# Optimization experiments

Hardware: AMD Instinct MI355X
Metric: run time of the kernel (lower is better)

The kernel has to match this reference:

```python
import jax, jax.numpy as jnp
import numpy as np

N = 100000   # num nodes
E = 1200000  # num edges
D = 64       # feature dim (input and both hidden layers)
R = 4        # num relations


def setup_inputs() -> dict:
    key = jax.random.key(0)
    ks = jax.random.split(key, 16)

    def p(k, shape, scale=0.05):
        return jax.random.normal(k, shape, dtype=jnp.float32) * scale

    inp = {
        "x": p(ks[0], (N, D), 1.0),
        "src": jax.random.randint(ks[1], (E,), 0, N),
        "dst": jax.random.randint(ks[2], (E,), 0, N),
        "rel": jax.random.randint(ks[3], (E,), 0, R),
    }
    i = 4
    for layer in (1, 2):
        inp[f"conv{layer}_w"] = p(ks[i], (D, R * D)); i += 1
        inp[f"conv{layer}_b"] = jnp.zeros((D,), jnp.float32)
        inp[f"conv{layer}_ws"] = p(ks[i], (D, D)); i += 1
        inp[f"conv{layer}_bs"] = jnp.zeros((D,), jnp.float32)
        inp[f"hw{layer}_pw"] = p(ks[i], (D, 2 * D)); i += 1
        inp[f"hw{layer}_pb"] = jnp.zeros((D,), jnp.float32)
        inp[f"hw{layer}_tw"] = p(ks[i], (D, 2 * D)); i += 1
        inp[f"hw{layer}_tb"] = jnp.full((D,), -2.0, jnp.float32)  # transform bias init -2
    return inp


def _rgc(x, src, dst, rel, w, b, ws, bs):
    # RelationalGraphConv: per-(node, relation) scatter-mean of source features,
    # then linear over concatenated relation slots + self-loop linear + sigmoid.
    msg = x[src]                                  # [E, D] gather
    seg = dst * R + rel                           # [E] flattened (node, relation) id
    s = jax.ops.segment_sum(msg, seg, num_segments=N * R)          # [N*R, D]
    cnt = jax.ops.segment_sum(jnp.ones((msg.shape[0], 1), msg.dtype), seg,
                              num_segments=N * R)                  # [N*R, 1]
    upd = (s / jnp.maximum(cnt, 1.0)).reshape(N, R * x.shape[1])   # [N, R*D]
    out = upd @ w.T + b + x @ ws.T + bs
    return jax.nn.sigmoid(out)


def _highway(h, prev, pw, pb, tw, tb):
    c = jnp.concatenate([h, prev], axis=1)        # [N, 2D]
    pr = jax.nn.relu(c @ pw.T + pb)
    g = jax.nn.sigmoid(c @ tw.T + tb)
    return g * pr + (1.0 - g) * h


def reference(x, src, dst, rel,
              conv1_w, conv1_b, conv1_ws, conv1_bs,
              hw1_pw, hw1_pb, hw1_tw, hw1_tb,
              conv2_w, conv2_b, conv2_ws, conv2_bs,
              hw2_pw, hw2_pb, hw2_tw, hw2_tb):
    h1 = _rgc(x, src, dst, rel, conv1_w, conv1_b, conv1_ws, conv1_bs)
    g1 = _highway(h1, x, hw1_pw, hw1_pb, hw1_tw, hw1_tb)   # prev_gcn = input
    h2 = _rgc(g1, src, dst, rel, conv2_w, conv2_b, conv2_ws, conv2_bs)
    g2 = _highway(h2, h1, hw2_pw, hw2_pb, hw2_tw, hw2_tb)  # prev_gcn = h1 (conv1 output)
    return g2  # node_feature, [N, D]
```

## Files before the change

### kernel.cpp

```cpp
#include <hip/hip_runtime.h>

#define NN 100000
#define NE 1200000
#define NRR 400000
#define NBIN 98
#define EPB 4096

typedef float f32x4 __attribute__((ext_vector_type(4)));
typedef __bf16 bf16x8 __attribute__((ext_vector_type(8)));

__device__ __forceinline__ float sigmoidf_(float x){ return 1.0f/(1.0f+__expf(-x)); }

__global__ __launch_bounds__(256)
void binhist_kernel(const int* __restrict__ dst, const int* __restrict__ rel,
                    int* __restrict__ bincnt){
  __shared__ int h[NBIN];
  int t = threadIdx.x;
  if (t < NBIN) h[t] = 0;
  __syncthreads();
  for (int e = blockIdx.x*256 + t; e < NE; e += 512*256){
    int bin = (dst[e]*4 + rel[e]) >> 12;
    atomicAdd(&h[bin], 1);
  }
  __syncthreads();
  if (t < NBIN && h[t]) atomicAdd(&bincnt[t], h[t]);
}

__global__ void binscan_kernel(const int* __restrict__ bincnt, int* __restrict__ binoff,
                               int* __restrict__ bincur, int* __restrict__ soff){
  if (threadIdx.x == 0){
    int s = 0;
    for (int i = 0; i < NBIN; ++i){ binoff[i] = s; bincur[i] = s; s += bincnt[i]; }
    binoff[NBIN] = NE;
    soff[NRR] = NE;
  }
}

__global__ __launch_bounds__(256)
void passA_kernel(const int* __restrict__ src, const int* __restrict__ dst,
                  const int* __restrict__ rel, int* __restrict__ bincur,
                  unsigned* __restrict__ ebin){
  __shared__ int h[NBIN], runbase[NBIN];
  int t = threadIdx.x;
  if (t < NBIN) h[t] = 0;
  __syncthreads();
  int lo = blockIdx.x*EPB, hi = min(lo + EPB, NE);
  for (int e = lo + t; e < hi; e += 256)
    atomicAdd(&h[(dst[e]*4 + rel[e]) >> 12], 1);
  __syncthreads();
  if (t < NBIN){
    runbase[t] = h[t] ? atomicAdd(&bincur[t], h[t]) : 0;
    h[t] = 0;
  }
  __syncthreads();
  for (int e = lo + t; e < hi; e += 256){
    int seg = dst[e]*4 + rel[e];
    int bin = seg >> 12;
    int p = runbase[bin] + atomicAdd(&h[bin], 1);
    ebin[p] = (unsigned)src[e] | ((unsigned)(seg & 4095) << 17);
  }
}

__global__ __launch_bounds__(1024)
void passB_kernel(const unsigned* __restrict__ ebin, const int* __restrict__ binoff,
                  int* __restrict__ soff, unsigned* __restrict__ ebuck){
  __shared__ int st[4096];
  __shared__ int wsum[16], wbase[16];
  const int bin = blockIdx.x;
  const int t = threadIdx.x;
  const int base = binoff[bin], end = binoff[bin+1];
  #pragma unroll
  for (int i = 0; i < 4; ++i) st[t*4 + i] = 0;
  __syncthreads();
  for (int e = base + t; e < end; e += 1024)
    atomicAdd(&st[(ebin[e] >> 17) & 4095], 1);
  __syncthreads();
  int h0 = st[t*4], h1 = st[t*4+1], h2 = st[t*4+2], h3 = st[t*4+3];
  int lsum = h0 + h1 + h2 + h3;
  int lane = t & 63, wv = t >> 6;
  int inc = lsum;
  #pragma unroll
  for (int o = 1; o < 64; o <<= 1){ int u = __shfl_up(inc, o); if (lane >= o) inc += u; }
  if (lane == 63) wsum[wv] = inc;
  __syncthreads();
  if (t == 0){ int s = 0; for (int i = 0; i < 16; ++i){ wbase[i] = s; s += wsum[i]; } }
  __syncthreads();
  int ex = base + wbase[wv] + (inc - lsum);
  int s0 = ex, s1 = ex + h0, s2 = s1 + h1, s3 = s2 + h2;
  st[t*4] = s0; st[t*4+1] = s1; st[t*4+2] = s2; st[t*4+3] = s3;
  int sg = bin*4096 + t*4;
  if (sg   < NRR) soff[sg]   = s0;
  if (sg+1 < NRR) soff[sg+1] = s1;
  if (sg+2 < NRR) soff[sg+2] = s2;
  if (sg+3 < NRR) soff[sg+3] = s3;
  __syncthreads();
  for (int e = base + t; e < end; e += 1024){
    unsigned u = ebin[e];
    int p = atomicAdd(&st[(u >> 17) & 4095], 1);
    ebuck[p] = u & 0x1FFFFu;
  }
}

__global__ void tobf16_kernel(const float* __restrict__ xf, __bf16* __restrict__ xb){
  int i = (blockIdx.x*256 + threadIdx.x)*8;
  if (i < NN*64){
    f32x4 a = *(const f32x4*)(xf + i);
    f32x4 b = *(const f32x4*)(xf + i + 4);
    bf16x8 r;
    r[0]=(__bf16)a[0]; r[1]=(__bf16)a[1]; r[2]=(__bf16)a[2]; r[3]=(__bf16)a[3];
    r[4]=(__bf16)b[0]; r[5]=(__bf16)b[1]; r[6]=(__bf16)b[2]; r[7]=(__bf16)b[3];
    *(bf16x8*)(xb + i) = r;
  }
}

__global__ void prep_kernel(const float* __restrict__ w,  const float* __restrict__ b,
                            const float* __restrict__ ws, const float* __restrict__ bs,
                            const float* __restrict__ pw, const float* __restrict__ pb,
                            const float* __restrict__ tw, const float* __restrict__ tb,
                            const float* __restrict__ w2,  const float* __restrict__ b2,
                            const float* __restrict__ ws2, const float* __restrict__ bs2,
                            const float* __restrict__ pw2, const float* __restrict__ pb2,
                            const float* __restrict__ tw2, const float* __restrict__ tb2,
                            __bf16* __restrict__ W1a, __bf16* __restrict__ W2a,
                            float* __restrict__ B1a, float* __restrict__ B2a,
                            __bf16* __restrict__ W1b, __bf16* __restrict__ W2b,
                            float* __restrict__ B1b, float* __restrict__ B2b){
  int i = blockIdx.x*256 + threadIdx.x;
  if (i < 64*320) {
    int e = i & 7, lane = (i >> 3) & 63, j = (i >> 9) & 3, kbi = i >> 11;
    int n = j*16 + (lane & 15);
    int k = kbi*32 + (lane >> 4)*8 + e;
    float va = (k < 256) ? w[n*256 + k]  : ws[n*64 + (k - 256)];
    float vb = (k < 256) ? w2[n*256 + k] : ws2[n*64 + (k - 256)];
    W1a[i] = (__bf16)va;
    W1b[i] = (__bf16)vb;
  }
  if (i < 128*128) {
    int e = i & 7, lane = (i >> 3) & 63, j = (i >> 9) & 7, kbi = i >> 12;
    int n = j*16 + (lane & 15);
    int k = kbi*32 + (lane >> 4)*8 + e;
    float va = (n < 64) ? pw[n*128 + k]  : tw[(n - 64)*128 + k];
    float vb = (n < 64) ? pw2[n*128 + k] : tw2[(n - 64)*128 + k];
    W2a[i] = (__bf16)va;
    W2b[i] = (__bf16)vb;
  }
  if (i < 64)  { B1a[i] = b[i] + bs[i];  B1b[i] = b2[i] + bs2[i]; }
  if (i < 128) { B2a[i] = (i < 64) ? pb[i] : tb[i-64];
                 B2b[i] = (i < 64) ? pb2[i] : tb2[i-64]; }
}

__global__ __launch_bounds__(256)
void gather_kernel(const unsigned* __restrict__ ebuck, const int* __restrict__ soff,
                   const __bf16* __restrict__ inb, __bf16* __restrict__ segb){
  const int sgg = blockIdx.x*32 + (threadIdx.x >> 3);
  const int fl  = threadIdx.x & 7;
  const int e0 = soff[sgg];
  const int e1 = soff[sgg + 1];
  const int c  = e1 - e0;

  f32x4 a0 = {0.f,0.f,0.f,0.f}, a1 = {0.f,0.f,0.f,0.f};
  f32x4 b0 = {0.f,0.f,0.f,0.f}, b1 = {0.f,0.f,0.f,0.f};
  int i = 0;
  for (; i + 2 <= c; i += 2){
    int s0 = (int)ebuck[e0 + i];
    int s1 = (int)ebuck[e0 + i + 1];
    bf16x8 v0 = *(const bf16x8*)(&inb[(size_t)s0*64 + fl*8]);
    bf16x8 v1 = *(const bf16x8*)(&inb[(size_t)s1*64 + fl*8]);
    a0[0]+=(float)v0[0]; a0[1]+=(float)v0[1]; a0[2]+=(float)v0[2]; a0[3]+=(float)v0[3];
    a1[0]+=(float)v0[4]; a1[1]+=(float)v0[5]; a1[2]+=(float)v0[6]; a1[3]+=(float)v0[7];
    b0[0]+=(float)v1[0]; b0[1]+=(float)v1[1]; b0[2]+=(float)v1[2]; b0[3]+=(float)v1[3];
    b1[0]+=(float)v1[4]; b1[1]+=(float)v1[5]; b1[2]+=(float)v1[6]; b1[3]+=(float)v1[7];
  }
  if (i < c){
    int s0 = (int)ebuck[e0 + i];
    bf16x8 v0 = *(const bf16x8*)(&inb[(size_t)s0*64 + fl*8]);
    a0[0]+=(float)v0[0]; a0[1]+=(float)v0[1]; a0[2]+=(float)v0[2]; a0[3]+=(float)v0[3];
    a1[0]+=(float)v0[4]; a1[1]+=(float)v0[5]; a1[2]+=(float)v0[6]; a1[3]+=(float)v0[7];
  }
  float inv = 1.0f / fmaxf((float)c, 1.0f);
  bf16x8 r;
  r[0]=(__bf16)((a0[0]+b0[0])*inv); r[1]=(__bf16)((a0[1]+b0[1])*inv);
  r[2]=(__bf16)((a0[2]+b0[2])*inv); r[3]=(__bf16)((a0[3]+b0[3])*inv);
  r[4]=(__bf16)((a1[0]+b1[0])*inv); r[5]=(__bf16)((a1[1]+b1[1])*inv);
  r[6]=(__bf16)((a1[2]+b1[2])*inv); r[7]=(__bf16)((a1[3]+b1[3])*inv);

  const int n   = sgg >> 2, rr = sgg & 3;
  const int nb  = n >> 4,  ml = n & 15;
  const int kbi = rr*2 + (fl >> 2);
  const int kgs = fl & 3;
  *(bf16x8*)(&segb[(size_t)((nb*8 + kbi)*64 + kgs*16 + ml)*8]) = r;
}

#define HSP 72

template<bool LAYER1>
__global__ __launch_bounds__(256, 4)
void dense_kernel(const __bf16* __restrict__ segbs,
                  const __bf16* __restrict__ xinb,
                  const __bf16* __restrict__ prevb,
                  const __bf16* __restrict__ W1s,
                  const __bf16* __restrict__ W2s,
                  const float* __restrict__ bias1,
                  const float* __restrict__ bias2,
                  __bf16* __restrict__ hb,
                  __bf16* __restrict__ gb,
                  float* __restrict__ outp)
{
  __shared__ __align__(16) __bf16 hs[64*HSP];
  __shared__ __align__(16) float outs[64*64];

  const int tid  = threadIdx.x;
  const int lane = tid & 63;
  const int wv   = tid >> 6;
  const int mloc = lane & 15;
  const int kg   = lane >> 4;
  const int wb   = blockIdx.x*64 + wv*16;
  const int arow = min(wb + mloc, NN-1);
  const int nbq  = min(wb, NN-16) >> 4;
  const size_t abase = (size_t)nbq * (8*512);

  f32x4 acc1[4] = {};

  #pragma unroll
  for (int kbi = 0; kbi < 8; ++kbi) {
    bf16x8 af = *(const bf16x8*)(&segbs[abase + (size_t)(kbi*64 + lane)*8]);
    #pragma unroll
    for (int j = 0; j < 4; ++j) {
      bf16x8 bf = *(const bf16x8*)(&W1s[((kbi*4 + j)*64 + lane)*8]);
      acc1[j] = __builtin_amdgcn_mfma_f32_16x16x32_bf16(af, bf, acc1[j], 0,0,0);
    }
  }
  #pragma unroll
  for (int kb = 0; kb < 64; kb += 32) {
    bf16x8 af = *(const bf16x8*)(&xinb[(size_t)arow*64 + kb + kg*8]);
    const int kbi = 8 + (kb >> 5);
    #pragma unroll
    for (int j = 0; j < 4; ++j) {
      bf16x8 bf = *(const bf16x8*)(&W1s[((kbi*4 + j)*64 + lane)*8]);
      acc1[j] = __builtin_amdgcn_mfma_f32_16x16x32_bf16(af, bf, acc1[j], 0,0,0);
    }
  }

  #pragma unroll
  for (int j = 0; j < 4; ++j) {
    int col = j*16 + mloc;
    float b1 = bias1[col];
    #pragma unroll
    for (int r = 0; r < 4; ++r) {
      float hv = sigmoidf_(acc1[j][r] + b1);
      acc1[j][r] = hv;
      hs[(wv*16 + kg*4 + r)*HSP + col] = (__bf16)hv;
    }
  }

  if (LAYER1) {
    #pragma unroll
    for (int i = 0; i < 2; ++i) {
      int r2 = i*8 + (lane >> 3);
      int c2 = lane & 7;
      bf16x8 v = *(const bf16x8*)(&hs[(wv*16 + r2)*HSP + c2*8]);
      int grow = wb + r2;
      if (grow < NN) *(bf16x8*)(&hb[(size_t)grow*64 + c2*8]) = v;
    }
  }

  f32x4 acc2[8] = {};
  #pragma unroll
  for (int kb = 0; kb < 64; kb += 32) {
    bf16x8 af = *(const bf16x8*)(&hs[(wv*16 + mloc)*HSP + kb + kg*8]);
    const int kbi = kb >> 5;
    #pragma unroll
    for (int j = 0; j < 8; ++j) {
      bf16x8 bf = *(const bf16x8*)(&W2s[((kbi*8 + j)*64 + lane)*8]);
      acc2[j] = __builtin_amdgcn_mfma_f32_16x16x32_bf16(af, bf, acc2[j], 0,0,0);
    }
  }
  #pragma unroll
  for (int kb = 0; kb < 64; kb += 32) {
    bf16x8 af = *(const bf16x8*)(&prevb[(size_t)arow*64 + kb + kg*8]);
    const int kbi = 2 + (kb >> 5);
    #pragma unroll
    for (int j = 0; j < 8; ++j) {
      bf16x8 bf = *(const bf16x8*)(&W2s[((kbi*8 + j)*64 + lane)*8]);
      acc2[j] = __builtin_amdgcn_mfma_f32_16x16x32_bf16(af, bf, acc2[j], 0,0,0);
    }
  }

  #pragma unroll
  for (int j = 0; j < 4; ++j) {
    int col = j*16 + mloc;
    float bp = bias2[col];
    float bt = bias2[64 + col];
    #pragma unroll
    for (int r = 0; r < 4; ++r) {
      float pr = fmaxf(acc2[j][r] + bp, 0.0f);
      float g  = sigmoidf_(acc2[j+4][r] + bt);
      float hv = acc1[j][r];
      float ov = g*pr + (1.0f - g)*hv;
      if (LAYER1) {
        hs[(wv*16 + kg*4 + r)*HSP + col] = (__bf16)ov;
      } else {
        outs[(wv*16 + kg*4 + r)*64 + col] = ov;
      }
    }
  }
  if (LAYER1) {
    #pragma unroll
    for (int i = 0; i < 2; ++i) {
      int r2 = i*8 + (lane >> 3);
      int c2 = lane & 7;
      bf16x8 v = *(const bf16x8*)(&hs[(wv*16 + r2)*HSP + c2*8]);
      int grow = wb + r2;
      if (grow < NN) *(bf16x8*)(&gb[(size_t)grow*64 + c2*8]) = v;
    }
  } else {
    #pragma unroll
    for (int i = 0; i < 4; ++i) {
      int pos = i*256 + lane*4;
      int r2 = pos >> 6, c2 = pos & 63;
      int grow = wb + r2;
      if (grow < NN)
        *(f32x4*)(&outp[(size_t)grow*64 + c2]) =
            *(const f32x4*)(&outs[(wv*16 + r2)*64 + c2]);
    }
  }
}

extern "C" void kernel_launch(void* const* d_in, const int* in_sizes, int n_in,
                              void* d_out, int out_size, void* d_ws, size_t ws_size,
                              hipStream_t stream){
  const float* x    = (const float*)d_in[0];
  const int*   src  = (const int*)d_in[1];
  const int*   dst  = (const int*)d_in[2];
  const int*   rel  = (const int*)d_in[3];
  const float* c1w  = (const float*)d_in[4];
  const float* c1b  = (const float*)d_in[5];
  const float* c1ws = (const float*)d_in[6];
  const float* c1bs = (const float*)d_in[7];
  const float* h1pw = (const float*)d_in[8];
  const float* h1pb = (const float*)d_in[9];
  const float* h1tw = (const float*)d_in[10];
  const float* h1tb = (const float*)d_in[11];
  const float* c2w  = (const float*)d_in[12];
  const float* c2b  = (const float*)d_in[13];
  const float* c2ws = (const float*)d_in[14];
  const float* c2bs = (const float*)d_in[15];
  const float* h2pw = (const float*)d_in[16];
  const float* h2pb = (const float*)d_in[17];
  const float* h2tw = (const float*)d_in[18];
  const float* h2tb = (const float*)d_in[19];

  char* p = (char*)d_ws;
  __bf16* segb = (__bf16*)p;  p += (size_t)NRR*64*2;
  __bf16* xb   = (__bf16*)p;  p += (size_t)NN*64*2;
  __bf16* h1b  = (__bf16*)p;  p += (size_t)NN*64*2;
  __bf16* g1b  = (__bf16*)p;  p += (size_t)NN*64*2;
  unsigned* ebuck = (unsigned*)p; p += (size_t)NE*4;
  unsigned* ebin  = (unsigned*)p; p += (size_t)NE*4;
  int* soff    = (int*)p;     p += (size_t)(NRR+8)*4;
  int* bincnt  = (int*)p;     p += 128*4;
  int* binoff  = (int*)p;     p += 128*4;
  int* bincur  = (int*)p;     p += 128*4;
  __bf16* W1a  = (__bf16*)p;  p += 64*320*2;
  __bf16* W2a  = (__bf16*)p;  p += 128*128*2;
  __bf16* W1b  = (__bf16*)p;  p += 64*320*2;
  __bf16* W2b  = (__bf16*)p;  p += 128*128*2;
  float* B1a   = (float*)p;   p += 64*4;
  float* B2a   = (float*)p;   p += 128*4;
  float* B1b   = (float*)p;   p += 64*4;
  float* B2b   = (float*)p;   p += 128*4;

  float* out = (float*)d_out;

  hipMemsetAsync(bincnt, 0, 128*4, stream);
  binhist_kernel<<<512, 256, 0, stream>>>(dst, rel, bincnt);
  binscan_kernel<<<1, 64, 0, stream>>>(bincnt, binoff, bincur, soff);
  passA_kernel<<<(NE+EPB-1)/EPB, 256, 0, stream>>>(src, dst, rel, bincur, ebin);
  passB_kernel<<<NBIN, 1024, 0, stream>>>(ebin, binoff, soff, ebuck);

  tobf16_kernel<<<(NN*64/8 + 255)/256, 256, 0, stream>>>(x, xb);
  prep_kernel<<<80, 256, 0, stream>>>(c1w, c1b, c1ws, c1bs, h1pw, h1pb, h1tw, h1tb,
                                      c2w, c2b, c2ws, c2bs, h2pw, h2pb, h2tw, h2tb,
                                      W1a, W2a, B1a, B2a, W1b, W2b, B1b, B2b);

  gather_kernel<<<NRR/32, 256, 0, stream>>>(ebuck, soff, xb, segb);
  dense_kernel<true><<<(NN+63)/64, 256, 0, stream>>>(segb, xb, xb, W1a, W2a, B1a, B2a,
                                                     h1b, g1b, nullptr);
  gather_kernel<<<NRR/32, 256, 0, stream>>>(ebuck, soff, g1b, segb);
  dense_kernel<false><<<(NN+63)/64, 256, 0, stream>>>(segb, g1b, h1b, W1b, W2b, B1b, B2b,
                                                      nullptr, nullptr, out);
}
```

Baseline: 298.4 us.

## Replace two-pass bin sort with global atomic counting sort, fuse prep kernels

Replaces the binning radix-style sort (binscan, passA, passB) with a per-segment global histogram built in binhist, a block-wise exclusive scan producing offsets and cursors, and a scatter kernel that places each edge via a global atomic on its segment cursor. The bf16 conversion and weight-prep kernels are merged into one launch, and the gather kernel preloads the first eight edge indices up front to raise memory-level parallelism. This cuts launches and one full pass over the edge array, at the cost of 1.2M contended global atomics and a non-deterministic edge order within each segment.

```diff
diff --git a/kernel.cpp b/kernel.cpp
--- a/kernel.cpp
+++ b/kernel.cpp
@@ -4,7 +4,6 @@
 #define NE 1200000
 #define NRR 400000
 #define NBIN 98
-#define EPB 4096
 
 typedef float f32x4 __attribute__((ext_vector_type(4)));
 typedef __bf16 bf16x8 __attribute__((ext_vector_type(8)));
@@ -13,69 +12,36 @@
 
 __global__ __launch_bounds__(256)
 void binhist_kernel(const int* __restrict__ dst, const int* __restrict__ rel,
-                    int* __restrict__ bincnt){
+                    int* __restrict__ bincnt, int* __restrict__ scnt){
   __shared__ int h[NBIN];
   int t = threadIdx.x;
   if (t < NBIN) h[t] = 0;
   __syncthreads();
   for (int e = blockIdx.x*256 + t; e < NE; e += 512*256){
-    int bin = (dst[e]*4 + rel[e]) >> 12;
-    atomicAdd(&h[bin], 1);
+    int seg = dst[e]*4 + rel[e];
+    atomicAdd(&scnt[seg], 1);
+    atomicAdd(&h[seg >> 12], 1);
   }
   __syncthreads();
   if (t < NBIN && h[t]) atomicAdd(&bincnt[t], h[t]);
 }
 
-__global__ void binscan_kernel(const int* __restrict__ bincnt, int* __restrict__ binoff,
-                               int* __restrict__ bincur, int* __restrict__ soff){
-  if (threadIdx.x == 0){
-    int s = 0;
-    for (int i = 0; i < NBIN; ++i){ binoff[i] = s; bincur[i] = s; s += bincnt[i]; }
-    binoff[NBIN] = NE;
-    soff[NRR] = NE;
-  }
-}
-
-__global__ __launch_bounds__(256)
-void passA_kernel(const int* __restrict__ src, const int* __restrict__ dst,
-                  const int* __restrict__ rel, int* __restrict__ bincur,
-                  unsigned* __restrict__ ebin){
-  __shared__ int h[NBIN], runbase[NBIN];
-  int t = threadIdx.x;
-  if (t < NBIN) h[t] = 0;
-  __syncthreads();
-  int lo = blockIdx.x*EPB, hi = min(lo + EPB, NE);
-  for (int e = lo + t; e < hi; e += 256)
-    atomicAdd(&h[(dst[e]*4 + rel[e]) >> 12], 1);
-  __syncthreads();
-  if (t < NBIN){
-    runbase[t] = h[t] ? atomicAdd(&bincur[t], h[t]) : 0;
-    h[t] = 0;
-  }
-  __syncthreads();
-  for (int e = lo + t; e < hi; e += 256){
-    int seg = dst[e]*4 + rel[e];
-    int bin = seg >> 12;
-    int p = runbase[bin] + atomicAdd(&h[bin], 1);
-    ebin[p] = (unsigned)src[e] | ((unsigned)(seg & 4095) << 17);
-  }
-}
-
 __global__ __launch_bounds__(1024)
-void passB_kernel(const unsigned* __restrict__ ebin, const int* __restrict__ binoff,
-                  int* __restrict__ soff, unsigned* __restrict__ ebuck){
-  __shared__ int st[4096];
-  __shared__ int wsum[16], wbase[16];
+void segscan_kernel(const int* __restrict__ bincnt, const int* __restrict__ scnt,
+                    int* __restrict__ soff, int* __restrict__ scur){
+  __shared__ int bc[NBIN];
+  __shared__ int wsum[16], wbase[16], bb;
   const int bin = blockIdx.x;
   const int t = threadIdx.x;
-  const int base = binoff[bin], end = binoff[bin+1];
-  #pragma unroll
-  for (int i = 0; i < 4; ++i) st[t*4 + i] = 0;
-  __syncthreads();
-  for (int e = base + t; e < end; e += 1024)
-    atomicAdd(&st[(ebin[e] >> 17) & 4095], 1);
-  __syncthreads();
-  int h0 = st[t*4], h1 = st[t*4+1], h2 = st[t*4+2], h3 = st[t*4+3];
+  if (t < NBIN) bc[t] = bincnt[t];
+  __syncthreads();
+  if (t == 0){ int s = 0; for (int i = 0; i < bin; ++i) s += bc[i]; bb = s; }
+  __syncthreads();
+  const int sg = bin*4096 + t*4;
+  int h0=0,h1=0,h2=0,h3=0;
+  if (sg < NRR){
+    h0 = scnt[sg]; h1 = scnt[sg+1]; h2 = scnt[sg+2]; h3 = scnt[sg+3];
+  }
   int lsum = h0 + h1 + h2 + h3;
   int lane = t & 63, wv = t >> 6;
   int inc = lsum;
@@ -85,47 +51,55 @@
   __syncthreads();
   if (t == 0){ int s = 0; for (int i = 0; i < 16; ++i){ wbase[i] = s; s += wsum[i]; } }
   __syncthreads();
-  int ex = base + wbase[wv] + (inc - lsum);
+  int ex = bb + wbase[wv] + (inc - lsum);
   int s0 = ex, s1 = ex + h0, s2 = s1 + h1, s3 = s2 + h2;
-  st[t*4] = s0; st[t*4+1] = s1; st[t*4+2] = s2; st[t*4+3] = s3;
-  int sg = bin*4096 + t*4;
-  if (sg   < NRR) soff[sg]   = s0;
-  if (sg+1 < NRR) soff[sg+1] = s1;
-  if (sg+2 < NRR) soff[sg+2] = s2;
-  if (sg+3 < NRR) soff[sg+3] = s3;
-  __syncthreads();
-  for (int e = base + t; e < end; e += 1024){
-    unsigned u = ebin[e];
-    int p = atomicAdd(&st[(u >> 17) & 4095], 1);
-    ebuck[p] = u & 0x1FFFFu;
-  }
-}
-
-__global__ void tobf16_kernel(const float* __restrict__ xf, __bf16* __restrict__ xb){
-  int i = (blockIdx.x*256 + threadIdx.x)*8;
-  if (i < NN*64){
-    f32x4 a = *(const f32x4*)(xf + i);
-    f32x4 b = *(const f32x4*)(xf + i + 4);
-    bf16x8 r;
-    r[0]=(__bf16)a[0]; r[1]=(__bf16)a[1]; r[2]=(__bf16)a[2]; r[3]=(__bf16)a[3];
-    r[4]=(__bf16)b[0]; r[5]=(__bf16)b[1]; r[6]=(__bf16)b[2]; r[7]=(__bf16)b[3];
-    *(bf16x8*)(xb + i) = r;
-  }
-}
-
-__global__ void prep_kernel(const float* __restrict__ w,  const float* __restrict__ b,
-                            const float* __restrict__ ws, const float* __restrict__ bs,
-                            const float* __restrict__ pw, const float* __restrict__ pb,
-                            const float* __restrict__ tw, const float* __restrict__ tb,
-                            const float* __restrict__ w2,  const float* __restrict__ b2,
-                            const float* __restrict__ ws2, const float* __restrict__ bs2,
-                            const float* __restrict__ pw2, const float* __restrict__ pb2,
-                            const float* __restrict__ tw2, const float* __restrict__ tb2,
-                            __bf16* __restrict__ W1a, __bf16* __restrict__ W2a,
-                            float* __restrict__ B1a, float* __restrict__ B2a,
-                            __bf16* __restrict__ W1b, __bf16* __restrict__ W2b,
-                            float* __restrict__ B1b, float* __restrict__ B2b){
-  int i = blockIdx.x*256 + threadIdx.x;
+  if (sg < NRR){
+    soff[sg] = s0; soff[sg+1] = s1; soff[sg+2] = s2; soff[sg+3] = s3;
+    scur[sg] = s0; scur[sg+1] = s1; scur[sg+2] = s2; scur[sg+3] = s3;
+  }
+  if (bin == NBIN-1 && t == 0) soff[NRR] = NE;
+}
+
+__global__ __launch_bounds__(256)
+void scatter_kernel(const int* __restrict__ src, const int* __restrict__ dst,
+                    const int* __restrict__ rel, int* __restrict__ scur,
+                    unsigned* __restrict__ ebuck){
+  int e = blockIdx.x*256 + threadIdx.x;
+  if (e < NE){
+    int seg = dst[e]*4 + rel[e];
+    int p = atomicAdd(&scur[seg], 1);
+    ebuck[p] = (unsigned)src[e];
+  }
+}
+
+#define TBB 3125
+__global__ __launch_bounds__(256)
+void tobf16_prep_kernel(const float* __restrict__ xf, __bf16* __restrict__ xb,
+                        const float* __restrict__ w,  const float* __restrict__ b,
+                        const float* __restrict__ ws, const float* __restrict__ bs,
+                        const float* __restrict__ pw, const float* __restrict__ pb,
+                        const float* __restrict__ tw, const float* __restrict__ tb,
+                        const float* __restrict__ w2,  const float* __restrict__ b2,
+                        const float* __restrict__ ws2, const float* __restrict__ bs2,
+                        const float* __restrict__ pw2, const float* __restrict__ pb2,
+                        const float* __restrict__ tw2, const float* __restrict__ tb2,
+                        __bf16* __restrict__ W1a, __bf16* __restrict__ W2a,
+                        float* __restrict__ B1a, float* __restrict__ B2a,
+                        __bf16* __restrict__ W1b, __bf16* __restrict__ W2b,
+                        float* __restrict__ B1b, float* __restrict__ B2b){
+  if (blockIdx.x < TBB) {
+    int i = (blockIdx.x*256 + threadIdx.x)*8;
+    if (i < NN*64){
+      f32x4 a = *(const f32x4*)(xf + i);
+      f32x4 c = *(const f32x4*)(xf + i + 4);
+      bf16x8 r;
+      r[0]=(__bf16)a[0]; r[1]=(__bf16)a[1]; r[2]=(__bf16)a[2]; r[3]=(__bf16)a[3];
+      r[4]=(__bf16)c[0]; r[5]=(__bf16)c[1]; r[6]=(__bf16)c[2]; r[7]=(__bf16)c[3];
+      *(bf16x8*)(xb + i) = r;
+    }
+    return;
+  }
+  int i = (blockIdx.x - TBB)*256 + threadIdx.x;
   if (i < 64*320) {
     int e = i & 7, lane = (i >> 3) & 63, j = (i >> 9) & 3, kbi = i >> 11;
     int n = j*16 + (lane & 15);
@@ -158,24 +132,36 @@
   const int e1 = soff[sgg + 1];
   const int c  = e1 - e0;
 
+  int idx[8];
+  #pragma unroll
+  for (int k = 0; k < 8; ++k) idx[k] = (int)ebuck[e0 + k];
+
   f32x4 a0 = {0.f,0.f,0.f,0.f}, a1 = {0.f,0.f,0.f,0.f};
   f32x4 b0 = {0.f,0.f,0.f,0.f}, b1 = {0.f,0.f,0.f,0.f};
-  int i = 0;
-  for (; i + 2 <= c; i += 2){
-    int s0 = (int)ebuck[e0 + i];
-    int s1 = (int)ebuck[e0 + i + 1];
-    bf16x8 v0 = *(const bf16x8*)(&inb[(size_t)s0*64 + fl*8]);
-    bf16x8 v1 = *(const bf16x8*)(&inb[(size_t)s1*64 + fl*8]);
-    a0[0]+=(float)v0[0]; a0[1]+=(float)v0[1]; a0[2]+=(float)v0[2]; a0[3]+=(float)v0[3];
-    a1[0]+=(float)v0[4]; a1[1]+=(float)v0[5]; a1[2]+=(float)v0[6]; a1[3]+=(float)v0[7];
-    b0[0]+=(float)v1[0]; b0[1]+=(float)v1[1]; b0[2]+=(float)v1[2]; b0[3]+=(float)v1[3];
-    b1[0]+=(float)v1[4]; b1[1]+=(float)v1[5]; b1[2]+=(float)v1[6]; b1[3]+=(float)v1[7];
-  }
-  if (i < c){
+  #pragma unroll
+  for (int k = 0; k < 8; ++k) {
+    if (k < c) {
+      bf16x8 v = *(const bf16x8*)(&inb[(size_t)idx[k]*64 + fl*8]);
+      if (k & 1) {
+        b0[0]+=(float)v[0]; b0[1]+=(float)v[1]; b0[2]+=(float)v[2]; b0[3]+=(float)v[3];
+        b1[0]+=(float)v[4]; b1[1]+=(float)v[5]; b1[2]+=(float)v[6]; b1[3]+=(float)v[7];
+      } else {
+        a0[0]+=(float)v[0]; a0[1]+=(float)v[1]; a0[2]+=(float)v[2]; a0[3]+=(float)v[3];
+        a1[0]+=(float)v[4]; a1[1]+=(float)v[5]; a1[2]+=(float)v[6]; a1[3]+=(float)v[7];
+      }
+    }
+  }
+  for (int i = 8; i < c; i += 2) {
     int s0 = (int)ebuck[e0 + i];
     bf16x8 v0 = *(const bf16x8*)(&inb[(size_t)s0*64 + fl*8]);
     a0[0]+=(float)v0[0]; a0[1]+=(float)v0[1]; a0[2]+=(float)v0[2]; a0[3]+=(float)v0[3];
     a1[0]+=(float)v0[4]; a1[1]+=(float)v0[5]; a1[2]+=(float)v0[6]; a1[3]+=(float)v0[7];
+    if (i + 1 < c) {
+      int s1 = (int)ebuck[e0 + i + 1];
+      bf16x8 v1 = *(const bf16x8*)(&inb[(size_t)s1*64 + fl*8]);
+      b0[0]+=(float)v1[0]; b0[1]+=(float)v1[1]; b0[2]+=(float)v1[2]; b0[3]+=(float)v1[3];
+      b1[0]+=(float)v1[4]; b1[1]+=(float)v1[5]; b1[2]+=(float)v1[6]; b1[3]+=(float)v1[7];
+    }
   }
   float inv = 1.0f / fmaxf((float)c, 1.0f);
   bf16x8 r;
@@ -355,12 +341,11 @@
   __bf16* xb   = (__bf16*)p;  p += (size_t)NN*64*2;
   __bf16* h1b  = (__bf16*)p;  p += (size_t)NN*64*2;
   __bf16* g1b  = (__bf16*)p;  p += (size_t)NN*64*2;
-  unsigned* ebuck = (unsigned*)p; p += (size_t)NE*4;
-  unsigned* ebin  = (unsigned*)p; p += (size_t)NE*4;
+  unsigned* ebuck = (unsigned*)p; p += (size_t)(NE+16)*4;
+  int* scnt    = (int*)p;     p += (size_t)(NRR+4096)*4;
+  int* bincnt  = (int*)p;     p += 128*4;
   int* soff    = (int*)p;     p += (size_t)(NRR+8)*4;
-  int* bincnt  = (int*)p;     p += 128*4;
-  int* binoff  = (int*)p;     p += 128*4;
-  int* bincur  = (int*)p;     p += 128*4;
+  int* scur    = (int*)p;     p += (size_t)NRR*4;
   __bf16* W1a  = (__bf16*)p;  p += 64*320*2;
   __bf16* W2a  = (__bf16*)p;  p += 128*128*2;
   __bf16* W1b  = (__bf16*)p;  p += 64*320*2;
@@ -372,14 +357,13 @@
 
   float* out = (float*)d_out;
 
-  hipMemsetAsync(bincnt, 0, 128*4, stream);
-  binhist_kernel<<<512, 256, 0, stream>>>(dst, rel, bincnt);
-  binscan_kernel<<<1, 64, 0, stream>>>(bincnt, binoff, bincur, soff);
-  passA_kernel<<<(NE+EPB-1)/EPB, 256, 0, stream>>>(src, dst, rel, bincur, ebin);
-  passB_kernel<<<NBIN, 1024, 0, stream>>>(ebin, binoff, soff, ebuck);
-
-  tobf16_kernel<<<(NN*64/8 + 255)/256, 256, 0, stream>>>(x, xb);
-  prep_kernel<<<80, 256, 0, stream>>>(c1w, c1b, c1ws, c1bs, h1pw, h1pb, h1tw, h1tb,
+  hipMemsetAsync(scnt, 0, ((size_t)(NRR+4096) + 128)*4, stream);
+  binhist_kernel<<<512, 256, 0, stream>>>(dst, rel, bincnt, scnt);
+  segscan_kernel<<<NBIN, 1024, 0, stream>>>(bincnt, scnt, soff, scur);
+  scatter_kernel<<<(NE+255)/256, 256, 0, stream>>>(src, dst, rel, scur, ebuck);
+
+  tobf16_prep_kernel<<<TBB+80, 256, 0, stream>>>(x, xb,
+                                      c1w, c1b, c1ws, c1bs, h1pw, h1pb, h1tw, h1tb,
                                       c2w, c2b, c2ws, c2bs, h2pw, h2pb, h2tw, h2tb,
                                       W1a, W2a, B1a, B2a, W1b, W2b, B1b, B2b);
 
```

Result: slower. 374.5 us (+25.5%).

## Fuse sort and prep kernels into one cooperative kernel with grid syncs

Applied to the files above, without the earlier changes.

Merges the bin histogram, bin scan, pass A scatter, pass B per-bin sort, bf16 conversion of x and weight packing into a single cooperative kernel of 98 blocks of 1024 threads, using grid-wide syncs in place of separate launches and a memset. Per-block partial histograms are written out and every block reduces and scans them redundantly. The aim is to remove launch overhead and inter-kernel gaps, at the cost of running the edge passes on only 98 blocks, which may underuse the GPU compared with the earlier wider grids.

```diff
diff --git a/kernel.cpp b/kernel.cpp
--- a/kernel.cpp
+++ b/kernel.cpp
@@ -1,74 +1,126 @@
 #include <hip/hip_runtime.h>
+#include <hip/hip_cooperative_groups.h>
+
+namespace cg = cooperative_groups;
 
 #define NN 100000
 #define NE 1200000
 #define NRR 400000
 #define NBIN 98
-#define EPB 4096
+#define CEPB 12245
 
 typedef float f32x4 __attribute__((ext_vector_type(4)));
 typedef __bf16 bf16x8 __attribute__((ext_vector_type(8)));
 
 __device__ __forceinline__ float sigmoidf_(float x){ return 1.0f/(1.0f+__expf(-x)); }
 
-__global__ __launch_bounds__(256)
-void binhist_kernel(const int* __restrict__ dst, const int* __restrict__ rel,
-                    int* __restrict__ bincnt){
-  __shared__ int h[NBIN];
-  int t = threadIdx.x;
-  if (t < NBIN) h[t] = 0;
-  __syncthreads();
-  for (int e = blockIdx.x*256 + t; e < NE; e += 512*256){
-    int bin = (dst[e]*4 + rel[e]) >> 12;
-    atomicAdd(&h[bin], 1);
-  }
-  __syncthreads();
-  if (t < NBIN && h[t]) atomicAdd(&bincnt[t], h[t]);
-}
-
-__global__ void binscan_kernel(const int* __restrict__ bincnt, int* __restrict__ binoff,
-                               int* __restrict__ bincur, int* __restrict__ soff){
-  if (threadIdx.x == 0){
+__global__ __launch_bounds__(1024)
+void sortprep_kernel(const int* __restrict__ src, const int* __restrict__ dst,
+                     const int* __restrict__ rel,
+                     const float* __restrict__ xf, __bf16* __restrict__ xb,
+                     const float* __restrict__ w,  const float* __restrict__ b,
+                     const float* __restrict__ ws, const float* __restrict__ bs,
+                     const float* __restrict__ pw, const float* __restrict__ pb,
+                     const float* __restrict__ tw, const float* __restrict__ tb,
+                     const float* __restrict__ w2,  const float* __restrict__ b2,
+                     const float* __restrict__ ws2, const float* __restrict__ bs2,
+                     const float* __restrict__ pw2, const float* __restrict__ pb2,
+                     const float* __restrict__ tw2, const float* __restrict__ tb2,
+                     __bf16* __restrict__ W1a, __bf16* __restrict__ W2a,
+                     float* __restrict__ B1a, float* __restrict__ B2a,
+                     __bf16* __restrict__ W1b, __bf16* __restrict__ W2b,
+                     float* __restrict__ B1b, float* __restrict__ B2b,
+                     int* __restrict__ hpart,
+                     unsigned* __restrict__ ebin, int* __restrict__ bincur,
+                     int* __restrict__ soff, unsigned* __restrict__ ebuck)
+{
+  cg::grid_group grid = cg::this_grid();
+  __shared__ int st[4096];
+  __shared__ int aux[NBIN + 2];
+  __shared__ int wsum[16], wbase[16];
+
+  const int t   = threadIdx.x;
+  const int bid = blockIdx.x;
+  const int lo  = bid*CEPB, hi = min(lo + CEPB, NE);
+
+  if (t < 128) st[t] = 0;
+  __syncthreads();
+  for (int e = lo + t; e < hi; e += 1024)
+    atomicAdd(&st[(dst[e]*4 + rel[e]) >> 12], 1);
+
+  for (int i = (bid*1024 + t)*8; i < NN*64; i += NBIN*1024*8){
+    f32x4 a = *(const f32x4*)(xf + i);
+    f32x4 c = *(const f32x4*)(xf + i + 4);
+    bf16x8 r;
+    r[0]=(__bf16)a[0]; r[1]=(__bf16)a[1]; r[2]=(__bf16)a[2]; r[3]=(__bf16)a[3];
+    r[4]=(__bf16)c[0]; r[5]=(__bf16)c[1]; r[6]=(__bf16)c[2]; r[7]=(__bf16)c[3];
+    *(bf16x8*)(xb + i) = r;
+  }
+  {
+    int i = bid*1024 + t;
+    if (i < 64*320) {
+      int e = i & 7, lane = (i >> 3) & 63, j = (i >> 9) & 3, kbi = i >> 11;
+      int n = j*16 + (lane & 15);
+      int k = kbi*32 + (lane >> 4)*8 + e;
+      float va = (k < 256) ? w[n*256 + k]  : ws[n*64 + (k - 256)];
+      float vb = (k < 256) ? w2[n*256 + k] : ws2[n*64 + (k - 256)];
+      W1a[i] = (__bf16)va;
+      W1b[i] = (__bf16)vb;
+    }
+    if (i < 128*128) {
+      int e = i & 7, lane = (i >> 3) & 63, j = (i >> 9) & 7, kbi = i >> 12;
+      int n = j*16 + (lane & 15);
+      int k = kbi*32 + (lane >> 4)*8 + e;
+      float va = (n < 64) ? pw[n*128 + k]  : tw[(n - 64)*128 + k];
+      float vb = (n < 64) ? pw2[n*128 + k] : tw2[(n - 64)*128 + k];
+      W2a[i] = (__bf16)va;
+      W2b[i] = (__bf16)vb;
+    }
+    if (i < 64)  { B1a[i] = b[i] + bs[i];  B1b[i] = b2[i] + bs2[i]; }
+    if (i < 128) { B2a[i] = (i < 64) ? pb[i] : tb[i-64];
+                   B2b[i] = (i < 64) ? pb2[i] : tb2[i-64]; }
+    if (i == 0) soff[NRR] = NE;
+  }
+  __syncthreads();
+  if (t < NBIN) hpart[bid*NBIN + t] = st[t];
+
+  grid.sync();
+
+  if (t < NBIN) {
     int s = 0;
-    for (int i = 0; i < NBIN; ++i){ binoff[i] = s; bincur[i] = s; s += bincnt[i]; }
-    binoff[NBIN] = NE;
-    soff[NRR] = NE;
-  }
-}
-
-__global__ __launch_bounds__(256)
-void passA_kernel(const int* __restrict__ src, const int* __restrict__ dst,
-                  const int* __restrict__ rel, int* __restrict__ bincur,
-                  unsigned* __restrict__ ebin){
-  __shared__ int h[NBIN], runbase[NBIN];
-  int t = threadIdx.x;
-  if (t < NBIN) h[t] = 0;
-  __syncthreads();
-  int lo = blockIdx.x*EPB, hi = min(lo + EPB, NE);
-  for (int e = lo + t; e < hi; e += 256)
-    atomicAdd(&h[(dst[e]*4 + rel[e]) >> 12], 1);
+    for (int k = 0; k < NBIN; ++k) s += hpart[k*NBIN + t];
+    st[t] = s;
+  }
+  __syncthreads();
+  if (t == 0) {
+    int s = 0;
+    for (int i = 0; i < NBIN; ++i){ aux[i] = s; s += st[i]; }
+    aux[NBIN] = NE;
+    bincur[bid] = aux[bid];
+  }
+
+  grid.sync();
+
+  if (t < 128) { st[t] = 0; }
+  __syncthreads();
+  for (int e = lo + t; e < hi; e += 1024)
+    atomicAdd(&st[(dst[e]*4 + rel[e]) >> 12], 1);
   __syncthreads();
   if (t < NBIN){
-    runbase[t] = h[t] ? atomicAdd(&bincur[t], h[t]) : 0;
-    h[t] = 0;
-  }
-  __syncthreads();
-  for (int e = lo + t; e < hi; e += 256){
+    st[128 + t] = st[t] ? atomicAdd(&bincur[t], st[t]) : 0;
+    st[t] = 0;
+  }
+  __syncthreads();
+  for (int e = lo + t; e < hi; e += 1024){
     int seg = dst[e]*4 + rel[e];
     int bin = seg >> 12;
-    int p = runbase[bin] + atomicAdd(&h[bin], 1);
+    int p = st[128 + bin] + atomicAdd(&st[bin], 1);
     ebin[p] = (unsigned)src[e] | ((unsigned)(seg & 4095) << 17);
   }
-}
-
-__global__ __launch_bounds__(1024)
-void passB_kernel(const unsigned* __restrict__ ebin, const int* __restrict__ binoff,
-                  int* __restrict__ soff, unsigned* __restrict__ ebuck){
-  __shared__ int st[4096];
-  __shared__ int wsum[16], wbase[16];
-  const int bin = blockIdx.x;
-  const int t = threadIdx.x;
-  const int base = binoff[bin], end = binoff[bin+1];
+
+  grid.sync();
+
+  const int base = aux[bid], end = aux[bid + 1];
   #pragma unroll
   for (int i = 0; i < 4; ++i) st[t*4 + i] = 0;
   __syncthreads();
@@ -88,7 +140,7 @@
   int ex = base + wbase[wv] + (inc - lsum);
   int s0 = ex, s1 = ex + h0, s2 = s1 + h1, s3 = s2 + h2;
   st[t*4] = s0; st[t*4+1] = s1; st[t*4+2] = s2; st[t*4+3] = s3;
-  int sg = bin*4096 + t*4;
+  int sg = bid*4096 + t*4;
   if (sg   < NRR) soff[sg]   = s0;
   if (sg+1 < NRR) soff[sg+1] = s1;
   if (sg+2 < NRR) soff[sg+2] = s2;
@@ -99,54 +151,6 @@
     int p = atomicAdd(&st[(u >> 17) & 4095], 1);
     ebuck[p] = u & 0x1FFFFu;
   }
-}
-
-__global__ void tobf16_kernel(const float* __restrict__ xf, __bf16* __restrict__ xb){
-  int i = (blockIdx.x*256 + threadIdx.x)*8;
-  if (i < NN*64){
-    f32x4 a = *(const f32x4*)(xf + i);
-    f32x4 b = *(const f32x4*)(xf + i + 4);
-    bf16x8 r;
-    r[0]=(__bf16)a[0]; r[1]=(__bf16)a[1]; r[2]=(__bf16)a[2]; r[3]=(__bf16)a[3];
-    r[4]=(__bf16)b[0]; r[5]=(__bf16)b[1]; r[6]=(__bf16)b[2]; r[7]=(__bf16)b[3];
-    *(bf16x8*)(xb + i) = r;
-  }
-}
-
-__global__ void prep_kernel(const float* __restrict__ w,  const float* __restrict__ b,
-                            const float* __restrict__ ws, const float* __restrict__ bs,
-                            const float* __restrict__ pw, const float* __restrict__ pb,
-                            const float* __restrict__ tw, const float* __restrict__ tb,
-                            const float* __restrict__ w2,  const float* __restrict__ b2,
-                            const float* __restrict__ ws2, const float* __restrict__ bs2,
-                            const float* __restrict__ pw2, const float* __restrict__ pb2,
-                            const float* __restrict__ tw2, const float* __restrict__ tb2,
-                            __bf16* __restrict__ W1a, __bf16* __restrict__ W2a,
-                            float* __restrict__ B1a, float* __restrict__ B2a,
-                            __bf16* __restrict__ W1b, __bf16* __restrict__ W2b,
-                            float* __restrict__ B1b, float* __restrict__ B2b){
-  int i = blockIdx.x*256 + threadIdx.x;
-  if (i < 64*320) {
-    int e = i & 7, lane = (i >> 3) & 63, j = (i >> 9) & 3, kbi = i >> 11;
-    int n = j*16 + (lane & 15);
-    int k = kbi*32 + (lane >> 4)*8 + e;
-    float va = (k < 256) ? w[n*256 + k]  : ws[n*64 + (k - 256)];
-    float vb = (k < 256) ? w2[n*256 + k] : ws2[n*64 + (k - 256)];
-    W1a[i] = (__bf16)va;
-    W1b[i] = (__bf16)vb;
-  }
-  if (i < 128*128) {
-    int e = i & 7, lane = (i >> 3) & 63, j = (i >> 9) & 7, kbi = i >> 12;
-    int n = j*16 + (lane & 15);
-    int k = kbi*32 + (lane >> 4)*8 + e;
-    float va = (n < 64) ? pw[n*128 + k]  : tw[(n - 64)*128 + k];
-    float vb = (n < 64) ? pw2[n*128 + k] : tw2[(n - 64)*128 + k];
-    W2a[i] = (__bf16)va;
-    W2b[i] = (__bf16)vb;
-  }
-  if (i < 64)  { B1a[i] = b[i] + bs[i];  B1b[i] = b2[i] + bs2[i]; }
-  if (i < 128) { B2a[i] = (i < 64) ? pb[i] : tb[i-64];
-                 B2b[i] = (i < 64) ? pb2[i] : tb2[i-64]; }
 }
 
 __global__ __launch_bounds__(256)
@@ -358,8 +362,7 @@
   unsigned* ebuck = (unsigned*)p; p += (size_t)NE*4;
   unsigned* ebin  = (unsigned*)p; p += (size_t)NE*4;
   int* soff    = (int*)p;     p += (size_t)(NRR+8)*4;
-  int* bincnt  = (int*)p;     p += 128*4;
-  int* binoff  = (int*)p;     p += 128*4;
+  int* hpart   = (int*)p;     p += (size_t)NBIN*NBIN*4;
   int* bincur  = (int*)p;     p += 128*4;
   __bf16* W1a  = (__bf16*)p;  p += 64*320*2;
   __bf16* W2a  = (__bf16*)p;  p += 128*128*2;
@@ -372,16 +375,19 @@
 
   float* out = (float*)d_out;
 
-  hipMemsetAsync(bincnt, 0, 128*4, stream);
-  binhist_kernel<<<512, 256, 0, stream>>>(dst, rel, bincnt);
-  binscan_kernel<<<1, 64, 0, stream>>>(bincnt, binoff, bincur, soff);
-  passA_kernel<<<(NE+EPB-1)/EPB, 256, 0, stream>>>(src, dst, rel, bincur, ebin);
-  passB_kernel<<<NBIN, 1024, 0, stream>>>(ebin, binoff, soff, ebuck);
-
-  tobf16_kernel<<<(NN*64/8 + 255)/256, 256, 0, stream>>>(x, xb);
-  prep_kernel<<<80, 256, 0, stream>>>(c1w, c1b, c1ws, c1bs, h1pw, h1pb, h1tw, h1tb,
-                                      c2w, c2b, c2ws, c2bs, h2pw, h2pb, h2tw, h2tb,
-                                      W1a, W2a, B1a, B2a, W1b, W2b, B1b, B2b);
+  void* args[] = {
+    (void*)&src, (void*)&dst, (void*)&rel,
+    (void*)&x, (void*)&xb,
+    (void*)&c1w, (void*)&c1b, (void*)&c1ws, (void*)&c1bs,
+    (void*)&h1pw, (void*)&h1pb, (void*)&h1tw, (void*)&h1tb,
+    (void*)&c2w, (void*)&c2b, (void*)&c2ws, (void*)&c2bs,
+    (void*)&h2pw, (void*)&h2pb, (void*)&h2tw, (void*)&h2tb,
+    (void*)&W1a, (void*)&W2a, (void*)&B1a, (void*)&B2a,
+    (void*)&W1b, (void*)&W2b, (void*)&B1b, (void*)&B2b,
+    (void*)&hpart, (void*)&ebin, (void*)&bincur, (void*)&soff, (void*)&ebuck
+  };
+  hipLaunchCooperativeKernel((void*)sortprep_kernel, dim3(NBIN), dim3(1024),
+                             args, 0, stream);
 
   gather_kernel<<<NRR/32, 256, 0, stream>>>(ebuck, soff, xb, segb);
   dense_kernel<true><<<(NN+63)/64, 256, 0, stream>>>(segb, xb, xb, W1a, W2a, B1a, B2a,
```

Result: slower. 363.6 us (+21.9%).
